# Performance work log

Hardware: AMD Instinct MI355X
Metric: run time of the kernel (lower is better)

## Reference

```python
import jax, jax.numpy as jnp
import numpy as np

CODE_NUM = 12288
GRAPH = 128      # graph_size: embedding width / GRU input
HIDDEN = 128     # GRU hidden = t_output_size = time_size (required by scatter/broadcast)
ATT = 64         # t_attention_size


def setup_inputs() -> dict:
    key = jax.random.key(0)
    ks = jax.random.split(key, 20)
    s = 0.05
    # disjoint 3-way membership masks (m1/m2/m3), some codes in no set
    cat = jax.random.randint(ks[0], (CODE_NUM,), 0, 4)
    divided = jax.nn.one_hot(cat, 4, dtype=jnp.int32)[:, :3]
    return {
        "interval": jnp.asarray(3.5, jnp.float32),
        "co_embeddings": jax.random.normal(ks[1], (CODE_NUM, GRAPH), jnp.float32),
        "no_embeddings": jax.random.normal(ks[2], (CODE_NUM, GRAPH), jnp.float32),
        "unrelated_embeddings": jax.random.normal(ks[3], (CODE_NUM, GRAPH), jnp.float32),
        "hidden_state": jax.random.normal(ks[4], (CODE_NUM, HIDDEN), jnp.float32),
        "divided": divided,
        # GRUCell params (torch layout: [3H, in], gates r|z|n)
        "W_ih": jax.random.normal(ks[5], (3 * HIDDEN, GRAPH), jnp.float32) * s,
        "W_hh": jax.random.normal(ks[6], (3 * HIDDEN, HIDDEN), jnp.float32) * s,
        "b_ih": jax.random.normal(ks[7], (3 * HIDDEN,), jnp.float32) * s,
        "b_hh": jax.random.normal(ks[8], (3 * HIDDEN,), jnp.float32) * s,
        # SingleHeadAttentionLayer params
        "Wq": jax.random.normal(ks[9], (ATT, GRAPH), jnp.float32) * s,
        "bq": jax.random.normal(ks[10], (ATT,), jnp.float32) * s,
        "Wk": jax.random.normal(ks[11], (ATT, GRAPH), jnp.float32) * s,
        "bk": jax.random.normal(ks[12], (ATT,), jnp.float32) * s,
        "Wv": jax.random.normal(ks[13], (HIDDEN, GRAPH), jnp.float32) * s,
        "bv": jax.random.normal(ks[14], (HIDDEN,), jnp.float32) * s,
        # time_layer: Linear(1, time_size)
        "Wt": jax.random.normal(ks[15], (HIDDEN, 1), jnp.float32) * s,
        "bt": jax.random.normal(ks[16], (HIDDEN,), jnp.float32) * s,
        "t": 1,
        "is_last": 0,
    }


def _gru_cell(x, h, W_ih, W_hh, b_ih, b_hh):
    gi = x @ W_ih.T + b_ih          # [N, 3H]
    gh = h @ W_hh.T + b_hh          # [N, 3H]
    i_r, i_z, i_n = jnp.split(gi, 3, axis=-1)
    h_r, h_z, h_n = jnp.split(gh, 3, axis=-1)
    r = jax.nn.sigmoid(i_r + h_r)
    z = jax.nn.sigmoid(i_z + h_z)
    n = jnp.tanh(i_n + r * h_n)
    return (1.0 - z) * n + z * h


def reference(interval, co_embeddings, no_embeddings, unrelated_embeddings,
              hidden_state, divided, W_ih, W_hh, b_ih, b_hh,
              Wq, bq, Wk, bk, Wv, bv, Wt, bt, t, is_last):
    dt = co_embeddings.dtype
    # time feature: tanh(Linear(1/log(interval + e)))
    x_t = 1.0 / jnp.log(interval + jnp.e)                       # scalar
    time_features = jnp.tanh(x_t * Wt[:, 0] + bt)               # [H]

    if is_last:
        out = _gru_cell(co_embeddings, hidden_state, W_ih, W_hh, b_ih, b_hh)
        return (out + time_features, None)

    m1 = divided[:, 0] > 0
    m2 = divided[:, 1] > 0
    m3 = divided[:, 2] > 0
    m23 = m2 | m3
    NEG = jnp.finfo(dt).min

    # --- m1 branch: GRUCell is row-wise, so compute on all rows and mask ---
    h_gru = _gru_cell(co_embeddings, hidden_state, W_ih, W_hh, b_ih, b_hh)  # [N, H]
    output_m1 = jnp.max(jnp.where(m1[:, None], h_gru, NEG), axis=0)        # [H]

    # --- m2/m3 branch: attention over the m23 subset (mask-based, order-free)
    # query rows: m2 -> no_embeddings, m3 -> unrelated_embeddings
    q_full = jnp.where(m2[:, None], no_embeddings, unrelated_embeddings)   # [N, G]
    Q = q_full @ Wq.T + bq                                                 # [N, A]
    K = co_embeddings @ Wk.T + bk                                          # [N, A]
    V = co_embeddings @ Wv.T + bv                                          # [N, H]
    scores = (Q @ K.T) / jnp.sqrt(jnp.asarray(ATT, dt))                    # [N, N]
    scores = jnp.where(m23[None, :], scores, NEG)                          # keys restricted to m23
    attn = jax.nn.softmax(scores, axis=-1)
    h_att = jnp.tanh(attn @ V)                                             # [N, H]
    output_m23 = jnp.max(jnp.where(m23[:, None], h_att, NEG), axis=0)      # [H]

    # scatter: m2/m3 rows written after m1 rows (m23 takes precedence)
    h_new = jnp.where(m23[:, None], h_att,
                      jnp.where(m1[:, None], h_gru, jnp.zeros((), dt)))

    output = jnp.maximum(output_m1, output_m23)
    return (output + time_features, h_new)
```

## Files before the change

### kernel.cpp

```cpp
#include <hip/hip_runtime.h>
#include <hip/hip_bf16.h>
#include <math.h>

#define N_CODES 12288
#define G 128
#define H 128
#define ATT 64
#define NEGF (-3.4028234663852886e38f)
#define NSEG 8
#define QT 128
#define NQT (N_CODES / QT)
#define QMAX 7168

typedef __attribute__((ext_vector_type(8))) short bf16x8;
typedef __attribute__((ext_vector_type(4))) float f32x4;
typedef __hip_bfloat16 bf16;
#define MFMA16(a, b, c) __builtin_amdgcn_mfma_f32_16x16x32_bf16(a, b, c, 0, 0, 0)

struct __align__(16) Ws {
  int n1;
  int n23;
  int pad_[2];
  int idx1[N_CODES];
  int rows23[N_CODES];
  int flags23[N_CODES];
  int inc[N_CODES];
  float tf[128];
  float part[256 * 128];
  float lseg[NSEG * QMAX];
  float bqkv[256];
  float b2[512];
  bf16 Wqkv[16 * 4 * 64 * 8];
  bf16 W2[32 * 8 * 64 * 8];
  bf16 Qb[(size_t)N_CODES * ATT];
  bf16 Kf[(size_t)N_CODES * ATT];
  bf16 Vf[(size_t)N_CODES * H];
  bf16 Oseg[(size_t)NSEG * QMAX * H];
};

__device__ inline uint2 pack4(float4 v) {
  union { bf16 b[4]; uint2 u; } cv;
  cv.b[0] = __float2bfloat16(v.x);
  cv.b[1] = __float2bfloat16(v.y);
  cv.b[2] = __float2bfloat16(v.z);
  cv.b[3] = __float2bfloat16(v.w);
  return cv.u;
}

__global__ void k_setup(const int* __restrict__ divided,
                        const float* __restrict__ Wq, const float* __restrict__ bq,
                        const float* __restrict__ Wk, const float* __restrict__ bk,
                        const float* __restrict__ Wv, const float* __restrict__ bv,
                        const float* __restrict__ W_ih, const float* __restrict__ W_hh,
                        const float* __restrict__ b_ih, const float* __restrict__ b_hh,
                        const float* __restrict__ interval, const float* __restrict__ Wt,
                        const float* __restrict__ bt, Ws* ws) {
  int bid = blockIdx.x;
  int t = threadIdx.x;
  if (bid < 48) {
    int r = bid * 256 + t;
    int m1 = divided[r * 3 + 0] > 0;
    int m2 = divided[r * 3 + 1] > 0;
    int m3 = divided[r * 3 + 2] > 0;
    ws->inc[r] = (m1 | m2 | m3);
    if (m1) {
      int p = atomicAdd(&ws->n1, 1);
      ws->idx1[p] = r;
    }
    if (m2 | m3) {
      int p = atomicAdd(&ws->n23, 1);
      ws->rows23[p] = r;
      ws->flags23[p] = m2;
    }
    return;
  }
  if (bid < 176) {
    int idx = (bid - 48) * 256 + t;
    int c = idx >> 7, k = idx & 127;
    float v;
    if (c < 64) v = Wq[c * G + k] * 0.125f;
    else if (c < 128) v = Wk[(c - 64) * G + k];
    else v = Wv[(c - 128) * G + k];
    int NB = c >> 4, lo = c & 15, ks = k >> 5, hi = (k >> 3) & 3, j = k & 7;
    ws->Wqkv[((NB * 4 + ks) * 64 + hi * 16 + lo) * 8 + j] = __float2bfloat16(v);
    return;
  }
  if (bid < 688) {
    int idx = (bid - 176) * 256 + t;
    int c = idx >> 8, k = idx & 255;
    int g = c >> 7, d = c & 127;
    float v = 0.f;
    if (g == 0) v = (k < 128) ? W_ih[d * G + k] : W_hh[d * H + (k - 128)];
    else if (g == 1) v = (k < 128) ? W_ih[(128 + d) * G + k] : W_hh[(128 + d) * H + (k - 128)];
    else if (g == 2) v = (k < 128) ? W_ih[(256 + d) * G + k] : 0.f;
    else v = (k < 128) ? 0.f : W_hh[(256 + d) * H + (k - 128)];
    int NB = c >> 4, lo = c & 15, ks = k >> 5, hi = (k >> 3) & 3, j = k & 7;
    ws->W2[((NB * 8 + ks) * 64 + hi * 16 + lo) * 8 + j] = __float2bfloat16(v);
    return;
  }
  if (t < 128) {
    float xt = 1.0f / logf(interval[0] + 2.718281828459045f);
    ws->tf[t] = tanhf(xt * Wt[t] + bt[t]);
  }
  for (int i = t; i < 768; i += 256) {
    if (i < 256) {
      float v;
      if (i < 64) v = bq[i] * 0.125f;
      else if (i < 128) v = bk[i - 64];
      else v = bv[i - 128];
      ws->bqkv[i] = v;
    } else {
      int c = i - 256;
      int g = c >> 7, d = c & 127;
      float v;
      if (g == 0) v = b_ih[d] + b_hh[d];
      else if (g == 1) v = b_ih[128 + d] + b_hh[128 + d];
      else if (g == 2) v = b_ih[256 + d];
      else v = b_hh[256 + d];
      ws->b2[c] = v;
    }
  }
}

__launch_bounds__(256)
__global__ void k_mm(const float* __restrict__ co, const float* __restrict__ no_e,
                     const float* __restrict__ un_e, const float* __restrict__ hs,
                     Ws* ws, float* __restrict__ h_new) {
  __shared__ __align__(16) bf16 sm[8704];
  int bid = blockIdx.x;
  int t = threadIdx.x;
  int w = t >> 6, lane = t & 63, lo = lane & 15, hi = lane >> 4;

  if (bid < 384) {
    int n23 = ws->n23;
    int q0 = bid * 32;
    if (q0 >= n23) return;
    bf16(*Aq)[136] = (bf16(*)[136])sm;
    bf16(*Ac)[136] = (bf16(*)[136])(sm + 4352);
    for (int it = 0; it < 4; ++it) {
      int idx = it * 256 + t;
      int rr = idx >> 5, c4 = idx & 31;
      uint2 pq = {0, 0}, pc = {0, 0};
      int p = q0 + rr;
      if (p < n23) {
        int row = ws->rows23[p];
        const float* srcq = ws->flags23[p] ? no_e : un_e;
        pq = pack4(*(const float4*)&srcq[(size_t)row * G + c4 * 4]);
        pc = pack4(*(const float4*)&co[(size_t)row * G + c4 * 4]);
      }
      *(uint2*)&Aq[rr][c4 * 4] = pq;
      *(uint2*)&Ac[rr][c4 * 4] = pc;
    }
    __syncthreads();
    const bf16(*At)[136] = (w == 0) ? Aq : Ac;
    f32x4 acc[2][4];
#pragma unroll
    for (int mf = 0; mf < 2; ++mf)
#pragma unroll
      for (int nb = 0; nb < 4; ++nb) acc[mf][nb] = (f32x4){0.f, 0.f, 0.f, 0.f};
#pragma unroll
    for (int ks = 0; ks < 4; ++ks) {
      bf16x8 af0 = *(const bf16x8*)&At[lo][ks * 32 + hi * 8];
      bf16x8 af1 = *(const bf16x8*)&At[16 + lo][ks * 32 + hi * 8];
#pragma unroll
      for (int nb = 0; nb < 4; ++nb) {
        bf16x8 bfr = *(const bf16x8*)&ws->Wqkv[(((w * 4 + nb) * 4 + ks) * 64 + lane) * 8];
        acc[0][nb] = MFMA16(af0, bfr, acc[0][nb]);
        acc[1][nb] = MFMA16(af1, bfr, acc[1][nb]);
      }
    }
#pragma unroll
    for (int mf = 0; mf < 2; ++mf) {
#pragma unroll
      for (int nb = 0; nb < 4; ++nb) {
        int c = w * 64 + nb * 16 + lo;
        float bias = ws->bqkv[c];
#pragma unroll
        for (int r = 0; r < 4; ++r) {
          int p = q0 + mf * 16 + hi * 4 + r;
          if (p >= n23) continue;
          bf16 bv16 = __float2bfloat16(acc[mf][nb][r] + bias);
          if (c < 64) {
            ws->Qb[(size_t)p * ATT + c] = bv16;
          } else if (c < 128) {
            int d = c - 64;
            ws->Kf[(((p >> 4) * 2 + (d >> 5)) * 64 + ((d >> 3) & 3) * 16 + (p & 15)) * 8 + (d & 7)] = bv16;
          } else {
            int d = c - 128;
            ws->Vf[((((p >> 6) * 8 + (d >> 4)) * 2 + ((p >> 5) & 1)) * 64 + ((p >> 3) & 3) * 16 + (d & 15)) * 8 + (p & 7)] = bv16;
          }
        }
      }
    }
  } else {
    int n1 = ws->n1;
    int q0 = (bid - 384) * 32;
    if (q0 >= n1) return;
    bf16(*A2)[264] = (bf16(*)[264])sm;
    for (int it = 0; it < 8; ++it) {
      int idx = it * 256 + t;
      int rr = idx >> 6, c4 = idx & 63;
      uint2 pk = {0, 0};
      int p = q0 + rr;
      if (p < n1) {
        int row = ws->idx1[p];
        float4 v = (c4 < 32) ? *(const float4*)&co[(size_t)row * G + c4 * 4]
                             : *(const float4*)&hs[(size_t)row * H + (c4 - 32) * 4];
        pk = pack4(v);
      }
      *(uint2*)&A2[rr][c4 * 4] = pk;
    }
    __syncthreads();
    f32x4 acc[2][8];
#pragma unroll
    for (int mf = 0; mf < 2; ++mf)
#pragma unroll
      for (int x = 0; x < 8; ++x) acc[mf][x] = (f32x4){0.f, 0.f, 0.f, 0.f};
#pragma unroll
    for (int ks = 0; ks < 8; ++ks) {
      bf16x8 af0 = *(const bf16x8*)&A2[lo][ks * 32 + hi * 8];
      bf16x8 af1 = *(const bf16x8*)&A2[16 + lo][ks * 32 + hi * 8];
#pragma unroll
      for (int g = 0; g < 4; ++g) {
#pragma unroll
        for (int nb2 = 0; nb2 < 2; ++nb2) {
          int NB = g * 8 + w * 2 + nb2;
          bf16x8 bfr = *(const bf16x8*)&ws->W2[((NB * 8 + ks) * 64 + lane) * 8];
          acc[0][g * 2 + nb2] = MFMA16(af0, bfr, acc[0][g * 2 + nb2]);
          acc[1][g * 2 + nb2] = MFMA16(af1, bfr, acc[1][g * 2 + nb2]);
        }
      }
    }
#pragma unroll
    for (int mf = 0; mf < 2; ++mf) {
#pragma unroll
      for (int nb2 = 0; nb2 < 2; ++nb2) {
        int d = w * 32 + nb2 * 16 + lo;
        float br = ws->b2[d], bz = ws->b2[128 + d], bin_ = ws->b2[256 + d], bhn = ws->b2[384 + d];
#pragma unroll
        for (int r = 0; r < 4; ++r) {
          int p = q0 + mf * 16 + hi * 4 + r;
          if (p >= n1) continue;
          int row = ws->idx1[p];
          float rs = acc[mf][0 + nb2][r] + br;
          float zs = acc[mf][2 + nb2][r] + bz;
          float in_ = acc[mf][4 + nb2][r] + bin_;
          float hn = acc[mf][6 + nb2][r] + bhn;
          float rg = 1.f / (1.f + __expf(-rs));
          float zg = 1.f / (1.f + __expf(-zs));
          float ng = tanhf(in_ + rg * hn);
          float h0 = hs[(size_t)row * H + d];
          h_new[(size_t)row * H + d] = (1.f - zg) * ng + zg * h0;
        }
      }
    }
  }
}

__launch_bounds__(256)
__global__ void k_attn(const Ws* __restrict__ ws, Ws* __restrict__ wso) {
  int n23 = ws->n23;
  int bid = blockIdx.x;
  int qi = bid % NQT;
  int rest = bid / NQT;
  int seg = rest & 7;
  int z = rest >> 3;
  int q0 = qi * QT;
  if (q0 >= n23) return;
  int segk = (((n23 + NSEG - 1) / NSEG) + 63) & ~63;
  int s0 = seg * segk;
  int t = threadIdx.x;
  if (s0 >= n23) {
    for (int idx = t; idx < QT * 64; idx += 256) {
      int q = q0 + (idx >> 6);
      if (q < n23)
        wso->Oseg[((size_t)seg * QMAX + q) * H + z * 64 + (idx & 63)] = __float2bfloat16(0.f);
    }
    if (z == 0 && t < QT && q0 + t < n23) wso->lseg[seg * QMAX + q0 + t] = 0.f;
    return;
  }
  int send = min(s0 + segk, n23);

  int w = t >> 6, lane = t & 63, lo = lane & 15, hi = lane >> 4;
  int qb = q0 + w * 32;

  __shared__ bf16 Pl[4][32][72];

  bf16x8 qf[2][2];
#pragma unroll
  for (int qs2 = 0; qs2 < 2; ++qs2)
#pragma unroll
    for (int s = 0; s < 2; ++s)
      qf[qs2][s] = *(const bf16x8*)&ws->Qb[(size_t)(qb + qs2 * 16 + lo) * ATT + s * 32 + hi * 8];

  f32x4 acc[2][4];
#pragma unroll
  for (int qs2 = 0; qs2 < 2; ++qs2)
#pragma unroll
    for (int ds = 0; ds < 4; ++ds) acc[qs2][ds] = (f32x4){0.f, 0.f, 0.f, 0.f};
  float l4[2][4] = {{0.f, 0.f, 0.f, 0.f}, {0.f, 0.f, 0.f, 0.f}};

  for (int c0 = s0; c0 < send; c0 += 64) {
    int kb0 = c0 >> 4;
    f32x4 sa[2][4];
#pragma unroll
    for (int j = 0; j < 4; ++j) {
      bf16x8 kf0 = *(const bf16x8*)&ws->Kf[(((kb0 + j) * 2 + 0) * 64 + lane) * 8];
      bf16x8 kf1 = *(const bf16x8*)&ws->Kf[(((kb0 + j) * 2 + 1) * 64 + lane) * 8];
#pragma unroll
      for (int qs2 = 0; qs2 < 2; ++qs2) {
        f32x4 s_ = {0.f, 0.f, 0.f, 0.f};
        s_ = MFMA16(qf[qs2][0], kf0, s_);
        s_ = MFMA16(qf[qs2][1], kf1, s_);
        sa[qs2][j] = s_;
      }
    }
#pragma unroll
    for (int j = 0; j < 4; ++j) {
      bool kv = (c0 + j * 16 + lo) < send;
#pragma unroll
      for (int qs2 = 0; qs2 < 2; ++qs2) {
#pragma unroll
        for (int r = 0; r < 4; ++r) {
          float p = kv ? __expf(sa[qs2][j][r]) : 0.f;
          l4[qs2][r] += p;
          Pl[w][qs2 * 16 + hi * 4 + r][j * 16 + lo] = __float2bfloat16(p);
        }
      }
    }
    int kc = c0 >> 6;
#pragma unroll
    for (int s = 0; s < 2; ++s) {
      bf16x8 pf0 = *(const bf16x8*)&Pl[w][lo][s * 32 + hi * 8];
      bf16x8 pf1 = *(const bf16x8*)&Pl[w][16 + lo][s * 32 + hi * 8];
#pragma unroll
      for (int ds = 0; ds < 4; ++ds) {
        bf16x8 vf = *(const bf16x8*)&ws->Vf[((kc * 16 + (z * 4 + ds) * 2 + s) * 64 + lane) * 8];
        acc[0][ds] = MFMA16(vf, pf0, acc[0][ds]);
        acc[1][ds] = MFMA16(vf, pf1, acc[1][ds]);
      }
    }
  }

  if (z == 0) {
#pragma unroll
    for (int qs2 = 0; qs2 < 2; ++qs2) {
#pragma unroll
      for (int r = 0; r < 4; ++r) {
        float l = l4[qs2][r];
#pragma unroll
        for (int off = 1; off < 16; off <<= 1) l += __shfl_xor(l, off);
        l4[qs2][r] = l;
      }
    }
    if (lo == 0) {
#pragma unroll
      for (int qs2 = 0; qs2 < 2; ++qs2)
#pragma unroll
        for (int r = 0; r < 4; ++r) {
          int q = qb + qs2 * 16 + hi * 4 + r;
          if (q < n23) wso->lseg[seg * QMAX + q] = l4[qs2][r];
        }
    }
  }
#pragma unroll
  for (int qs2 = 0; qs2 < 2; ++qs2) {
    int q = qb + qs2 * 16 + lo;
    if (q < n23) {
#pragma unroll
      for (int ds = 0; ds < 4; ++ds) {
        union { bf16 b[4]; uint2 u; } tmp;
#pragma unroll
        for (int r = 0; r < 4; ++r) tmp.b[r] = __float2bfloat16(acc[qs2][ds][r]);
        *(uint2*)&wso->Oseg[((size_t)seg * QMAX + q) * H + (z * 4 + ds) * 16 + hi * 4] = tmp.u;
      }
    }
  }
}

__global__ void k_merge(const Ws* __restrict__ ws, float* __restrict__ h_new) {
  int t = threadIdx.x;
  int q = blockIdx.x * 2 + (t >> 7);
  if (q >= ws->n23) return;
  int d = t & 127;
  float o = 0.f, L = 0.f;
#pragma unroll
  for (int s = 0; s < NSEG; ++s) {
    o += __bfloat162float(ws->Oseg[((size_t)s * QMAX + q) * H + d]);
    L += ws->lseg[s * QMAX + q];
  }
  h_new[(size_t)ws->rows23[q] * H + d] = tanhf(o / L);
}

__global__ void k_colmax(const Ws* __restrict__ ws, const float* __restrict__ h_new,
                         Ws* ws_out) {
  int h = threadIdx.x;
  int r0 = blockIdx.x * 48;
  float mx = NEGF;
  for (int r = 0; r < 48; ++r) {
    int row = r0 + r;
    if (ws->inc[row]) mx = fmaxf(mx, h_new[(size_t)row * H + h]);
  }
  ws_out->part[blockIdx.x * 128 + h] = mx;
}

__global__ void k_final(const Ws* __restrict__ ws, float* __restrict__ out) {
  __shared__ float red[256];
  int t = threadIdx.x;
  int h = t & 127, g = t >> 7;
  float mx = NEGF;
  for (int b = g; b < 256; b += 2) mx = fmaxf(mx, ws->part[b * 128 + h]);
  red[t] = mx;
  __syncthreads();
  if (t < 128) out[t] = fmaxf(red[t], red[t + 128]) + ws->tf[t];
}

extern "C" void kernel_launch(void* const* d_in, const int* in_sizes, int n_in,
                              void* d_out, int out_size, void* d_ws, size_t ws_size,
                              hipStream_t stream) {
  const float* interval = (const float*)d_in[0];
  const float* co = (const float*)d_in[1];
  const float* no_e = (const float*)d_in[2];
  const float* un_e = (const float*)d_in[3];
  const float* hs = (const float*)d_in[4];
  const int* divided = (const int*)d_in[5];
  const float* W_ih = (const float*)d_in[6];
  const float* W_hh = (const float*)d_in[7];
  const float* b_ih = (const float*)d_in[8];
  const float* b_hh = (const float*)d_in[9];
  const float* Wq = (const float*)d_in[10];
  const float* bq = (const float*)d_in[11];
  const float* Wk = (const float*)d_in[12];
  const float* bk = (const float*)d_in[13];
  const float* Wv = (const float*)d_in[14];
  const float* bv = (const float*)d_in[15];
  const float* Wt = (const float*)d_in[16];
  const float* bt = (const float*)d_in[17];

  float* out = (float*)d_out;
  float* h_new = out + 128;
  Ws* ws = (Ws*)d_ws;

  hipMemsetAsync(d_out, 0, (size_t)out_size * sizeof(float), stream);
  hipMemsetAsync(ws, 0, 16, stream);

  k_setup<<<689, 256, 0, stream>>>(divided, Wq, bq, Wk, bk, Wv, bv, W_ih, W_hh, b_ih, b_hh,
                                   interval, Wt, bt, ws);
  k_mm<<<768, 256, 0, stream>>>(co, no_e, un_e, hs, ws, h_new);
  k_attn<<<NQT * NSEG * 2, 256, 0, stream>>>(ws, ws);
  k_merge<<<QMAX / 2, 256, 0, stream>>>(ws, h_new);
  k_colmax<<<256, 128, 0, stream>>>(ws, h_new, ws);
  k_final<<<1, 256, 0, stream>>>(ws, out);
}
```

Before: 223.5 us.

## Restructure attention tiling and fuse column max into GRU and merge kernels

The attention kernel drops its two-way split of output columns. Each block now handles 64 queries against all 128 value columns, with the four waves sharing exponentiated scores through LDS, so the QK^T product is no longer computed twice. The column-max reduction is folded into the GRU epilogue and the merge kernel using order-preserving integer atomicMax, which removes the separate colmax pass and its h_new re-read. The cost is extra block-level syncs per key chunk and atomic contention on 128 counters.

Result: faster. 194.6 us (-12.9%).

```diff
diff --git a/kernel.cpp b/kernel.cpp
--- a/kernel.cpp
+++ b/kernel.cpp
@@ -8,7 +8,7 @@
 #define ATT 64
 #define NEGF (-3.4028234663852886e38f)
 #define NSEG 8
-#define QT 128
+#define QT 64
 #define NQT (N_CODES / QT)
 #define QMAX 7168
 
@@ -24,9 +24,8 @@
   int idx1[N_CODES];
   int rows23[N_CODES];
   int flags23[N_CODES];
-  int inc[N_CODES];
+  unsigned maxu[128];
   float tf[128];
-  float part[256 * 128];
   float lseg[NSEG * QMAX];
   float bqkv[256];
   float b2[512];
@@ -45,6 +44,21 @@
   cv.b[2] = __float2bfloat16(v.z);
   cv.b[3] = __float2bfloat16(v.w);
   return cv.u;
+}
+
+__device__ inline float bf2f(short s) {
+  union { unsigned u; float f; } c;
+  c.u = ((unsigned)(unsigned short)s) << 16;
+  return c.f;
+}
+
+__device__ inline unsigned fkey(float f) {
+  unsigned b = __float_as_uint(f);
+  return (b & 0x80000000u) ? ~b : (b | 0x80000000u);
+}
+__device__ inline float funkey(unsigned u) {
+  unsigned b = (u & 0x80000000u) ? (u & 0x7fffffffu) : ~u;
+  return __uint_as_float(b);
 }
 
 __global__ void k_setup(const int* __restrict__ divided,
@@ -62,7 +76,6 @@
     int m1 = divided[r * 3 + 0] > 0;
     int m2 = divided[r * 3 + 1] > 0;
     int m3 = divided[r * 3 + 2] > 0;
-    ws->inc[r] = (m1 | m2 | m3);
     if (m1) {
       int p = atomicAdd(&ws->n1, 1);
       ws->idx1[p] = r;
@@ -101,6 +114,7 @@
   if (t < 128) {
     float xt = 1.0f / logf(interval[0] + 2.718281828459045f);
     ws->tf[t] = tanhf(xt * Wt[t] + bt[t]);
+    ws->maxu[t] = 0u;
   }
   for (int i = t; i < 768; i += 256) {
     if (i < 256) {
@@ -231,6 +245,7 @@
         }
       }
     }
+    float mx2[2] = {NEGF, NEGF};
 #pragma unroll
     for (int mf = 0; mf < 2; ++mf) {
 #pragma unroll
@@ -250,9 +265,18 @@
           float zg = 1.f / (1.f + __expf(-zs));
           float ng = tanhf(in_ + rg * hn);
           float h0 = hs[(size_t)row * H + d];
-          h_new[(size_t)row * H + d] = (1.f - zg) * ng + zg * h0;
+          float hv = (1.f - zg) * ng + zg * h0;
+          h_new[(size_t)row * H + d] = hv;
+          mx2[nb2] = fmaxf(mx2[nb2], hv);
         }
       }
+    }
+#pragma unroll
+    for (int nb2 = 0; nb2 < 2; ++nb2) {
+      float m = mx2[nb2];
+      m = fmaxf(m, __shfl_xor(m, 16));
+      m = fmaxf(m, __shfl_xor(m, 32));
+      if (hi == 0) atomicMax(&ws->maxu[w * 32 + nb2 * 16 + lo], fkey(m));
     }
   }
 }
@@ -261,158 +285,138 @@
 __global__ void k_attn(const Ws* __restrict__ ws, Ws* __restrict__ wso) {
   int n23 = ws->n23;
   int bid = blockIdx.x;
-  int qi = bid % NQT;
-  int rest = bid / NQT;
-  int seg = rest & 7;
-  int z = rest >> 3;
-  int q0 = qi * QT;
+  int q0 = (bid % NQT) * QT;
+  int seg = bid / NQT;
   if (q0 >= n23) return;
   int segk = (((n23 + NSEG - 1) / NSEG) + 63) & ~63;
   int s0 = seg * segk;
   int t = threadIdx.x;
   if (s0 >= n23) {
-    for (int idx = t; idx < QT * 64; idx += 256) {
-      int q = q0 + (idx >> 6);
-      if (q < n23)
-        wso->Oseg[((size_t)seg * QMAX + q) * H + z * 64 + (idx & 63)] = __float2bfloat16(0.f);
-    }
-    if (z == 0 && t < QT && q0 + t < n23) wso->lseg[seg * QMAX + q0 + t] = 0.f;
+    for (int idx = t; idx < QT * 32; idx += 256) {
+      int q = q0 + (idx >> 5);
+      if (q < n23) {
+        uint2 z2 = {0, 0};
+        *(uint2*)&wso->Oseg[((size_t)seg * QMAX + q) * H + (idx & 31) * 4] = z2;
+      }
+    }
+    if (t < QT && q0 + t < n23) wso->lseg[seg * QMAX + q0 + t] = 0.f;
     return;
   }
   int send = min(s0 + segk, n23);
 
   int w = t >> 6, lane = t & 63, lo = lane & 15, hi = lane >> 4;
-  int qb = q0 + w * 32;
-
-  __shared__ bf16 Pl[4][32][72];
-
-  bf16x8 qf[2][2];
-#pragma unroll
-  for (int qs2 = 0; qs2 < 2; ++qs2)
+
+  __shared__ bf16 Pl[64][72];
+
+  bf16x8 qf[4][2];
+#pragma unroll
+  for (int qsub = 0; qsub < 4; ++qsub)
 #pragma unroll
     for (int s = 0; s < 2; ++s)
-      qf[qs2][s] = *(const bf16x8*)&ws->Qb[(size_t)(qb + qs2 * 16 + lo) * ATT + s * 32 + hi * 8];
+      qf[qsub][s] =
+          *(const bf16x8*)&ws->Qb[(size_t)(q0 + qsub * 16 + lo) * ATT + s * 32 + hi * 8];
 
   f32x4 acc[2][4];
 #pragma unroll
-  for (int qs2 = 0; qs2 < 2; ++qs2)
-#pragma unroll
-    for (int ds = 0; ds < 4; ++ds) acc[qs2][ds] = (f32x4){0.f, 0.f, 0.f, 0.f};
-  float l4[2][4] = {{0.f, 0.f, 0.f, 0.f}, {0.f, 0.f, 0.f, 0.f}};
+  for (int ddl = 0; ddl < 2; ++ddl)
+#pragma unroll
+    for (int qsub = 0; qsub < 4; ++qsub) acc[ddl][qsub] = (f32x4){0.f, 0.f, 0.f, 0.f};
+  float lacc = 0.f;
 
   for (int c0 = s0; c0 < send; c0 += 64) {
-    int kb0 = c0 >> 4;
-    f32x4 sa[2][4];
-#pragma unroll
-    for (int j = 0; j < 4; ++j) {
-      bf16x8 kf0 = *(const bf16x8*)&ws->Kf[(((kb0 + j) * 2 + 0) * 64 + lane) * 8];
-      bf16x8 kf1 = *(const bf16x8*)&ws->Kf[(((kb0 + j) * 2 + 1) * 64 + lane) * 8];
-#pragma unroll
-      for (int qs2 = 0; qs2 < 2; ++qs2) {
-        f32x4 s_ = {0.f, 0.f, 0.f, 0.f};
-        s_ = MFMA16(qf[qs2][0], kf0, s_);
-        s_ = MFMA16(qf[qs2][1], kf1, s_);
-        sa[qs2][j] = s_;
-      }
-    }
-#pragma unroll
-    for (int j = 0; j < 4; ++j) {
-      bool kv = (c0 + j * 16 + lo) < send;
-#pragma unroll
-      for (int qs2 = 0; qs2 < 2; ++qs2) {
-#pragma unroll
-        for (int r = 0; r < 4; ++r) {
-          float p = kv ? __expf(sa[qs2][j][r]) : 0.f;
-          l4[qs2][r] += p;
-          Pl[w][qs2 * 16 + hi * 4 + r][j * 16 + lo] = __float2bfloat16(p);
-        }
-      }
-    }
+    int kb = (c0 >> 4) + w;
+    bf16x8 kf0 = *(const bf16x8*)&ws->Kf[((size_t)(kb * 2 + 0) * 64 + lane) * 8];
+    bf16x8 kf1 = *(const bf16x8*)&ws->Kf[((size_t)(kb * 2 + 1) * 64 + lane) * 8];
+    bool kv = (c0 + w * 16 + lo) < send;
+#pragma unroll
+    for (int qsub = 0; qsub < 4; ++qsub) {
+      f32x4 s_ = {0.f, 0.f, 0.f, 0.f};
+      s_ = MFMA16(qf[qsub][0], kf0, s_);
+      s_ = MFMA16(qf[qsub][1], kf1, s_);
+#pragma unroll
+      for (int r = 0; r < 4; ++r) {
+        float p = kv ? __expf(s_[r]) : 0.f;
+        Pl[qsub * 16 + hi * 4 + r][w * 16 + lo] = __float2bfloat16(p);
+      }
+    }
+    __syncthreads();
+
     int kc = c0 >> 6;
 #pragma unroll
     for (int s = 0; s < 2; ++s) {
-      bf16x8 pf0 = *(const bf16x8*)&Pl[w][lo][s * 32 + hi * 8];
-      bf16x8 pf1 = *(const bf16x8*)&Pl[w][16 + lo][s * 32 + hi * 8];
-#pragma unroll
-      for (int ds = 0; ds < 4; ++ds) {
-        bf16x8 vf = *(const bf16x8*)&ws->Vf[((kc * 16 + (z * 4 + ds) * 2 + s) * 64 + lane) * 8];
-        acc[0][ds] = MFMA16(vf, pf0, acc[0][ds]);
-        acc[1][ds] = MFMA16(vf, pf1, acc[1][ds]);
-      }
-    }
-  }
-
-  if (z == 0) {
-#pragma unroll
-    for (int qs2 = 0; qs2 < 2; ++qs2) {
-#pragma unroll
-      for (int r = 0; r < 4; ++r) {
-        float l = l4[qs2][r];
-#pragma unroll
-        for (int off = 1; off < 16; off <<= 1) l += __shfl_xor(l, off);
-        l4[qs2][r] = l;
-      }
-    }
-    if (lo == 0) {
-#pragma unroll
-      for (int qs2 = 0; qs2 < 2; ++qs2)
-#pragma unroll
-        for (int r = 0; r < 4; ++r) {
-          int q = qb + qs2 * 16 + hi * 4 + r;
-          if (q < n23) wso->lseg[seg * QMAX + q] = l4[qs2][r];
-        }
-    }
-  }
-#pragma unroll
-  for (int qs2 = 0; qs2 < 2; ++qs2) {
-    int q = qb + qs2 * 16 + lo;
+      bf16x8 pf[4];
+#pragma unroll
+      for (int qsub = 0; qsub < 4; ++qsub)
+        pf[qsub] = *(const bf16x8*)&Pl[qsub * 16 + lo][s * 32 + hi * 8];
+#pragma unroll
+      for (int ddl = 0; ddl < 2; ++ddl) {
+        bf16x8 vf =
+            *(const bf16x8*)&ws->Vf[((size_t)(kc * 16 + (w * 2 + ddl) * 2 + s) * 64 + lane) * 8];
+#pragma unroll
+        for (int qsub = 0; qsub < 4; ++qsub) acc[ddl][qsub] = MFMA16(vf, pf[qsub], acc[ddl][qsub]);
+      }
+    }
+    {
+      bf16x8 pa = *(const bf16x8*)&Pl[w * 16 + lo][hi * 16];
+      bf16x8 pb = *(const bf16x8*)&Pl[w * 16 + lo][hi * 16 + 8];
+      float sl = 0.f;
+#pragma unroll
+      for (int j = 0; j < 8; ++j) sl += bf2f(pa[j]) + bf2f(pb[j]);
+      sl += __shfl_xor(sl, 16);
+      sl += __shfl_xor(sl, 32);
+      lacc += sl;
+    }
+    __syncthreads();
+  }
+
+  if (hi == 0) {
+    int q = q0 + w * 16 + lo;
+    if (q < n23) wso->lseg[seg * QMAX + q] = lacc;
+  }
+#pragma unroll
+  for (int qsub = 0; qsub < 4; ++qsub) {
+    int q = q0 + qsub * 16 + lo;
     if (q < n23) {
 #pragma unroll
-      for (int ds = 0; ds < 4; ++ds) {
+      for (int ddl = 0; ddl < 2; ++ddl) {
         union { bf16 b[4]; uint2 u; } tmp;
 #pragma unroll
-        for (int r = 0; r < 4; ++r) tmp.b[r] = __float2bfloat16(acc[qs2][ds][r]);
-        *(uint2*)&wso->Oseg[((size_t)seg * QMAX + q) * H + (z * 4 + ds) * 16 + hi * 4] = tmp.u;
-      }
-    }
-  }
-}
-
-__global__ void k_merge(const Ws* __restrict__ ws, float* __restrict__ h_new) {
+        for (int r = 0; r < 4; ++r) tmp.b[r] = __float2bfloat16(acc[ddl][qsub][r]);
+        *(uint2*)&wso->Oseg[((size_t)seg * QMAX + q) * H + w * 32 + ddl * 16 + hi * 4] = tmp.u;
+      }
+    }
+  }
+}
+
+__global__ void k_merge(const Ws* __restrict__ ws, float* __restrict__ h_new, Ws* wso) {
+  int n23 = ws->n23;
+  int qb = blockIdx.x * 32;
+  if (qb >= n23) return;
   int t = threadIdx.x;
-  int q = blockIdx.x * 2 + (t >> 7);
-  if (q >= ws->n23) return;
-  int d = t & 127;
-  float o = 0.f, L = 0.f;
-#pragma unroll
-  for (int s = 0; s < NSEG; ++s) {
-    o += __bfloat162float(ws->Oseg[((size_t)s * QMAX + q) * H + d]);
-    L += ws->lseg[s * QMAX + q];
-  }
-  h_new[(size_t)ws->rows23[q] * H + d] = tanhf(o / L);
-}
-
-__global__ void k_colmax(const Ws* __restrict__ ws, const float* __restrict__ h_new,
-                         Ws* ws_out) {
-  int h = threadIdx.x;
-  int r0 = blockIdx.x * 48;
+  int d = t & 127, half = t >> 7;
   float mx = NEGF;
-  for (int r = 0; r < 48; ++r) {
-    int row = r0 + r;
-    if (ws->inc[row]) mx = fmaxf(mx, h_new[(size_t)row * H + h]);
-  }
-  ws_out->part[blockIdx.x * 128 + h] = mx;
-}
-
-__global__ void k_final(const Ws* __restrict__ ws, float* __restrict__ out) {
+  for (int qi = 0; qi < 16; ++qi) {
+    int q = qb + half * 16 + qi;
+    if (q >= n23) break;
+    float o = 0.f, L = 0.f;
+#pragma unroll
+    for (int s = 0; s < NSEG; ++s) {
+      o += bf2f(((const short*)ws->Oseg)[((size_t)s * QMAX + q) * H + d]);
+      L += ws->lseg[s * QMAX + q];
+    }
+    float h = tanhf(o / L);
+    h_new[(size_t)ws->rows23[q] * H + d] = h;
+    mx = fmaxf(mx, h);
+  }
   __shared__ float red[256];
-  int t = threadIdx.x;
-  int h = t & 127, g = t >> 7;
-  float mx = NEGF;
-  for (int b = g; b < 256; b += 2) mx = fmaxf(mx, ws->part[b * 128 + h]);
   red[t] = mx;
   __syncthreads();
-  if (t < 128) out[t] = fmaxf(red[t], red[t + 128]) + ws->tf[t];
+  if (t < 128) atomicMax(&wso->maxu[t], fkey(fmaxf(red[t], red[t + 128])));
+}
+
+__global__ void k_final(const Ws* __restrict__ ws, float* __restrict__ out) {
+  int h = threadIdx.x;
+  out[h] = funkey(ws->maxu[h]) + ws->tf[h];
 }
 
 extern "C" void kernel_launch(void* const* d_in, const int* in_sizes, int n_in,
@@ -447,8 +451,7 @@
   k_setup<<<689, 256, 0, stream>>>(divided, Wq, bq, Wk, bk, Wv, bv, W_ih, W_hh, b_ih, b_hh,
                                    interval, Wt, bt, ws);
   k_mm<<<768, 256, 0, stream>>>(co, no_e, un_e, hs, ws, h_new);
-  k_attn<<<NQT * NSEG * 2, 256, 0, stream>>>(ws, ws);
-  k_merge<<<QMAX / 2, 256, 0, stream>>>(ws, h_new);
-  k_colmax<<<256, 128, 0, stream>>>(ws, h_new, ws);
-  k_final<<<1, 256, 0, stream>>>(ws, out);
-}
+  k_attn<<<NQT * NSEG, 256, 0, stream>>>(ws, ws);
+  k_merge<<<QMAX / 32, 256, 0, stream>>>(ws, h_new, ws);
+  k_final<<<1, 128, 0, stream>>>(ws, out);
+}
```
